# Kernel optimization log

Hardware: AMD Instinct MI355X
Metric: run time of the kernel (lower is better)

The kernel has to match this reference:

```python
import jax, jax.numpy as jnp
import numpy as np

N_NODES = 100000
K_HOPS = 2


def _gcn_norm(edge_index, edge_weight, num_nodes, fill_value=1.0):
    # renorm trick: add self-loops with weight fill_value, then D^-1/2 A D^-1/2
    row, col = edge_index[0], edge_index[1]
    sl = jnp.arange(num_nodes, dtype=edge_index.dtype)
    row = jnp.concatenate([row, sl])
    col = jnp.concatenate([col, sl])
    w = jnp.concatenate([edge_weight, jnp.full((num_nodes,), fill_value, edge_weight.dtype)])
    deg = jax.ops.segment_sum(w, row, num_segments=num_nodes)
    dinv = jnp.where(deg > 0, jax.lax.rsqrt(deg), 0.0)
    normed_w = dinv[row] * w * dinv[col]
    return row, col, normed_w


def setup_inputs() -> dict:
    key = jax.random.key(0)
    k1, k2, k3 = jax.random.split(key, 3)
    n_edges, d, units = 1000000, 64, 64
    x = jax.random.normal(k1, (N_NODES, d), dtype=jnp.float32)
    edge_index = jax.random.randint(k2, (2, n_edges), 0, N_NODES, dtype=jnp.int32)
    edge_weight = jnp.ones((n_edges,), dtype=jnp.float32)
    kernel = jax.random.normal(k3, (d, units), dtype=jnp.float32) * (1.0 / np.sqrt(d))
    bias = jnp.zeros((units,), dtype=jnp.float32)
    return {"x": x, "edge_index": edge_index, "edge_weight": edge_weight,
            "kernel": kernel, "bias": bias}


def reference(x, edge_index, edge_weight, kernel, bias):
    # SGC: K-hop normalized sparse propagation, then single dense linear
    row, col, w = _gcn_norm(edge_index, edge_weight, N_NODES, fill_value=1.0)
    h = x
    for _ in range(K_HOPS):
        h = jax.ops.segment_sum(w[:, None] * h[col], row, num_segments=N_NODES)
    out = h @ kernel + bias  # activation=None
    return out
```

## Files before the change

### kernel.cpp

```cpp
#include <hip/hip_runtime.h>


constexpr int kN = 100000;
constexpr int kD = 64;
constexpr int BSHIFT = 9;
constexpr int NBUCK = (kN + 511) >> BSHIFT;
constexpr int CHUNK = 4096;
constexpr int XW_ROWS = 128;
constexpr int ECW_PAD = 256;

__device__ __forceinline__ float bf2f(unsigned short u) {
    return __uint_as_float(((unsigned)u) << 16);
}
__device__ __forceinline__ unsigned short f2bf(float f) {
    unsigned b = __float_as_uint(f);
    b += 0x7FFF + ((b >> 16) & 1);
    return (unsigned short)(b >> 16);
}

__global__ __launch_bounds__(256) void k_xw_count(const float* __restrict__ x,
                                                  const float* __restrict__ W,
                                                  unsigned short* __restrict__ y,
                                                  const int* __restrict__ row,
                                                  int* __restrict__ bc,
                                                  int nxw, int nblk, int n, int E) {
    __shared__ float Xs[XW_ROWS][kD];
    int bid = blockIdx.x;
    int t = threadIdx.x;
    if (bid >= nxw) {
        int cb = bid - nxw;
        int* hist = (int*)&Xs[0][0];
        hist[t] = 0;
        __syncthreads();
        int g0 = cb * CHUNK;
        int nn = min(CHUNK, E - g0);
        for (int i = t; i < nn; i += 256) {
            atomicAdd(&hist[row[g0 + i] >> BSHIFT], 1);
        }
        __syncthreads();
        if (t < NBUCK) bc[t * nblk + cb] = hist[t];
        return;
    }
    int lane = t & 63;
    int wv = t >> 6;
    int row0 = bid * XW_ROWS;
    float Wc[kD];
#pragma unroll
    for (int k = 0; k < kD; ++k) Wc[k] = W[k * kD + lane];
    for (int i = t; i < XW_ROWS * (kD / 4); i += 256) {
        int r = i >> 4;
        int q = i & 15;
        float4 v = make_float4(0.0f, 0.0f, 0.0f, 0.0f);
        if (row0 + r < n)
            v = *reinterpret_cast<const float4*>(x + (size_t)(row0 + r) * kD + q * 4);
        *reinterpret_cast<float4*>(&Xs[r][q * 4]) = v;
    }
    __syncthreads();
    int rbase = wv * 32;
#pragma unroll
    for (int rr = 0; rr < 32; rr += 2) {
        int r0 = rbase + rr;
        float acc0 = 0.0f, acc1 = 0.0f;
#pragma unroll
        for (int q = 0; q < 16; ++q) {
            float4 a = *reinterpret_cast<const float4*>(&Xs[r0][q * 4]);
            float4 b = *reinterpret_cast<const float4*>(&Xs[r0 + 1][q * 4]);
            acc0 = fmaf(a.x, Wc[q * 4 + 0], acc0);
            acc1 = fmaf(b.x, Wc[q * 4 + 0], acc1);
            acc0 = fmaf(a.y, Wc[q * 4 + 1], acc0);
            acc1 = fmaf(b.y, Wc[q * 4 + 1], acc1);
            acc0 = fmaf(a.z, Wc[q * 4 + 2], acc0);
            acc1 = fmaf(b.z, Wc[q * 4 + 2], acc1);
            acc0 = fmaf(a.w, Wc[q * 4 + 3], acc0);
            acc1 = fmaf(b.w, Wc[q * 4 + 3], acc1);
        }
        int gr = row0 + r0;
        if (gr < n) y[(size_t)gr * kD + lane] = f2bf(acc0);
        if (gr + 1 < n) y[(size_t)(gr + 1) * kD + lane] = f2bf(acc1);
    }
}

__global__ __launch_bounds__(256) void kA_scanB(int* __restrict__ bc,
                                                int* __restrict__ tot, int nblk) {
    __shared__ int sh[256];
    int b = blockIdx.x;
    int t = threadIdx.x;
    int* p = bc + (size_t)b * nblk;
    int ipt = (nblk + 255) >> 8;
    int s0 = t * ipt;
    int s1 = min(s0 + ipt, nblk);
    int lsum = 0;
    for (int k = s0; k < s1; ++k) lsum += p[k];
    sh[t] = lsum;
    __syncthreads();
    for (int off = 1; off < 256; off <<= 1) {
        int add = (t >= off) ? sh[t - off] : 0;
        __syncthreads();
        sh[t] += add;
        __syncthreads();
    }
    int run = sh[t] - lsum;
    for (int k = s0; k < s1; ++k) {
        int v = p[k];
        p[k] = run;
        run += v;
    }
    if (t == 255) tot[b] = sh[255];
}

__global__ __launch_bounds__(256) void kA_scanT(const int* __restrict__ tot,
                                                int* __restrict__ base,
                                                int2* __restrict__ ecw_pad) {
    __shared__ int sh[256];
    int t = threadIdx.x;
    int v = (t < NBUCK) ? tot[t] : 0;
    sh[t] = v;
    __syncthreads();
    for (int off = 1; off < 256; off <<= 1) {
        int add = (t >= off) ? sh[t - off] : 0;
        __syncthreads();
        sh[t] += add;
        __syncthreads();
    }
    if (t < NBUCK) base[t] = sh[t] - v;
    ecw_pad[t] = make_int2(0, 0);
}

__global__ __launch_bounds__(256) void kA_place(const int* __restrict__ row,
                                                const int* __restrict__ col,
                                                const float* __restrict__ w,
                                                const int* __restrict__ bc,
                                                const int* __restrict__ base, int nblk,
                                                int2* __restrict__ tmp, int E) {
    __shared__ int hist[256];
    __shared__ int lbase[256];
    __shared__ int gb[256];
    __shared__ int cur[256];
    __shared__ int2 stage[CHUNK];
    __shared__ unsigned char bkt[CHUNK];
    int t = threadIdx.x;
    hist[t] = 0;
    __syncthreads();
    int g0 = blockIdx.x * CHUNK;
    int n = min(CHUNK, E - g0);
    for (int i = t; i < n; i += 256) {
        atomicAdd(&hist[row[g0 + i] >> BSHIFT], 1);
    }
    __syncthreads();
    int v = hist[t];
    lbase[t] = v;
    __syncthreads();
    for (int off = 1; off < 256; off <<= 1) {
        int add = (t >= off) ? lbase[t - off] : 0;
        __syncthreads();
        lbase[t] += add;
        __syncthreads();
    }
    int excl = lbase[t] - v;
    __syncthreads();
    lbase[t] = excl;
    cur[t] = excl;
    if (t < NBUCK) gb[t] = base[t] + bc[t * nblk + blockIdx.x];
    __syncthreads();
    for (int i = t; i < n; i += 256) {
        int r = row[g0 + i];
        int c = col[g0 + i];
        float wv = w[g0 + i];
        int b = r >> BSHIFT;
        int lp = atomicAdd(&cur[b], 1);
        stage[lp] = make_int2(c | ((r & 511) << 17), __float_as_int(wv));
        bkt[lp] = (unsigned char)b;
    }
    __syncthreads();
    for (int i = t; i < n; i += 256) {
        int b = bkt[i];
        tmp[gb[b] + (i - lbase[b])] = stage[i];
    }
}

__global__ __launch_bounds__(512) void kD_deg(const int2* __restrict__ tmp,
                                              const int* __restrict__ base,
                                              float* __restrict__ dinv, int E) {
    __shared__ float degs[512];
    int b = blockIdx.x;
    int t = threadIdx.x;
    degs[t] = 0.0f;
    __syncthreads();
    int gbase = base[b];
    int gend = (b == NBUCK - 1) ? E : base[b + 1];
    int node0 = b << BSHIFT;
    int nloc = min(512, kN - node0);
    for (int i = gbase + t; i < gend; i += 512) {
        int2 e = tmp[i];
        atomicAdd(&degs[(e.x >> 17) & 511], __int_as_float(e.y));
    }
    __syncthreads();
    if (t < nloc) {
        float d = 1.0f + degs[t];
        dinv[node0 + t] = (d > 0.0f) ? rsqrtf(d) : 0.0f;
    }
}

__global__ __launch_bounds__(512) void kB_sort(const int2* __restrict__ tmp,
                                               const int* __restrict__ base,
                                               const float* __restrict__ dinv,
                                               int2* __restrict__ ecw,
                                               int* __restrict__ start, int E) {
    __shared__ int hist[512];
    __shared__ int cur[512];
    int b = blockIdx.x;
    int t = threadIdx.x;
    int gbase = base[b];
    int gend = (b == NBUCK - 1) ? E : base[b + 1];
    int size = gend - gbase;
    int node0 = b << BSHIFT;
    int nloc = min(512, kN - node0);
    hist[t] = 0;
    __syncthreads();
    for (int i = t; i < size; i += 512) {
        atomicAdd(&hist[(tmp[gbase + i].x >> 17) & 511], 1);
    }
    __syncthreads();
    int v = hist[t];
    hist[t] = v;
    __syncthreads();
    for (int off = 1; off < 512; off <<= 1) {
        int add = (t >= off) ? hist[t - off] : 0;
        __syncthreads();
        hist[t] += add;
        __syncthreads();
    }
    int excl = hist[t] - v;
    __syncthreads();
    cur[t] = excl;
    __syncthreads();
    if (t < nloc) start[node0 + t] = gbase + excl;
    if (b == 0 && t == 0) start[kN] = E;
    for (int i = t; i < size; i += 512) {
        int2 e = tmp[gbase + i];
        int c = e.x & 0x1FFFF;
        int rl = (e.x >> 17) & 511;
        float wn = dinv[node0 + rl] * __int_as_float(e.y) * dinv[c];
        int lp = atomicAdd(&cur[rl], 1);
        ecw[gbase + lp] = make_int2(c << 7, __float_as_int(wn));
    }
}

template <typename OutWriter>
__device__ __forceinline__ void hop_body(const int* __restrict__ start,
                                         const int2* __restrict__ ecw,
                                         const float* __restrict__ dinv,
                                         const unsigned short* __restrict__ h_in,
                                         int n, OutWriter writeout) {
    int wv = threadIdx.x >> 6;
    int lane = threadIdx.x & 63;
    int q = lane >> 4;
    int f = lane & 15;
    int node = blockIdx.x * 16 + wv * 4 + q;
    bool valid = node < n;
    int nd = valid ? node : (n - 1);
    const char* hb = (const char*)h_in;
    int lo = f << 3;
    float di = dinv[nd];
    float d2 = di * di;
    uint2 su = *(const uint2*)(hb + ((size_t)nd << 7) + lo);
    float acc0 = d2 * __uint_as_float(su.x << 16);
    float acc1 = d2 * __uint_as_float(su.x & 0xffff0000u);
    float acc2 = d2 * __uint_as_float(su.y << 16);
    float acc3 = d2 * __uint_as_float(su.y & 0xffff0000u);
    int s = start[nd], e = start[nd + 1];
    int d = e - s;
    int m1 = max(d, __shfl_xor(d, 16));
    int dmax = max(m1, __shfl_xor(m1, 32));
    for (int it = 0; it < dmax; it += 4) {
        int j = s + it;
        int2 v0 = ecw[j + 0];
        int2 v1 = ecw[j + 1];
        int2 v2 = ecw[j + 2];
        int2 v3 = ecw[j + 3];
        uint2 g0 = *(const uint2*)(hb + (unsigned)(v0.x + lo));
        uint2 g1 = *(const uint2*)(hb + (unsigned)(v1.x + lo));
        uint2 g2 = *(const uint2*)(hb + (unsigned)(v2.x + lo));
        uint2 g3 = *(const uint2*)(hb + (unsigned)(v3.x + lo));
        float w0 = (it + 0 < d) ? __int_as_float(v0.y) : 0.0f;
        float w1 = (it + 1 < d) ? __int_as_float(v1.y) : 0.0f;
        float w2 = (it + 2 < d) ? __int_as_float(v2.y) : 0.0f;
        float w3 = (it + 3 < d) ? __int_as_float(v3.y) : 0.0f;
        acc0 = fmaf(w0, __uint_as_float(g0.x << 16), acc0);
        acc1 = fmaf(w0, __uint_as_float(g0.x & 0xffff0000u), acc1);
        acc2 = fmaf(w0, __uint_as_float(g0.y << 16), acc2);
        acc3 = fmaf(w0, __uint_as_float(g0.y & 0xffff0000u), acc3);
        acc0 = fmaf(w1, __uint_as_float(g1.x << 16), acc0);
        acc1 = fmaf(w1, __uint_as_float(g1.x & 0xffff0000u), acc1);
        acc2 = fmaf(w1, __uint_as_float(g1.y << 16), acc2);
        acc3 = fmaf(w1, __uint_as_float(g1.y & 0xffff0000u), acc3);
        acc0 = fmaf(w2, __uint_as_float(g2.x << 16), acc0);
        acc1 = fmaf(w2, __uint_as_float(g2.x & 0xffff0000u), acc1);
        acc2 = fmaf(w2, __uint_as_float(g2.y << 16), acc2);
        acc3 = fmaf(w2, __uint_as_float(g2.y & 0xffff0000u), acc3);
        acc0 = fmaf(w3, __uint_as_float(g3.x << 16), acc0);
        acc1 = fmaf(w3, __uint_as_float(g3.x & 0xffff0000u), acc1);
        acc2 = fmaf(w3, __uint_as_float(g3.y << 16), acc2);
        acc3 = fmaf(w3, __uint_as_float(g3.y & 0xffff0000u), acc3);
    }
    if (valid) writeout(node, f, acc0, acc1, acc2, acc3);
}

__global__ __launch_bounds__(256) void k_hop1(const int* __restrict__ start,
                                              const int2* __restrict__ ecw,
                                              const float* __restrict__ dinv,
                                              const unsigned short* __restrict__ h_in,
                                              uint2* __restrict__ h_out64, int n) {
    hop_body(start, ecw, dinv, h_in, n,
             [=](int node, int f, float a0, float a1, float a2, float a3) {
                 uint2 p;
                 p.x = (unsigned)f2bf(a0) | ((unsigned)f2bf(a1) << 16);
                 p.y = (unsigned)f2bf(a2) | ((unsigned)f2bf(a3) << 16);
                 h_out64[((size_t)node << 4) + f] = p;
             });
}

__global__ __launch_bounds__(256) void k_hop2(const int* __restrict__ start,
                                              const int2* __restrict__ ecw,
                                              const float* __restrict__ dinv,
                                              const unsigned short* __restrict__ h_in,
                                              const float* __restrict__ bias,
                                              float* __restrict__ out, int n) {
    hop_body(start, ecw, dinv, h_in, n,
             [=](int node, int f, float a0, float a1, float a2, float a3) {
                 float4 b = *reinterpret_cast<const float4*>(bias + (f << 2));
                 float4 o = make_float4(a0 + b.x, a1 + b.y, a2 + b.z, a3 + b.w);
                 *reinterpret_cast<float4*>(out + ((size_t)node << 6) + (f << 2)) = o;
             });
}

extern "C" void kernel_launch(void* const* d_in, const int* in_sizes, int n_in,
                              void* d_out, int out_size, void* d_ws, size_t ws_size,
                              hipStream_t stream) {
    const float* x    = (const float*)d_in[0];
    const int*   ei   = (const int*)d_in[1];
    const float* ew   = (const float*)d_in[2];
    const float* W    = (const float*)d_in[3];
    const float* bias = (const float*)d_in[4];
    const int E = in_sizes[1] / 2;
    const int* row = ei;
    const int* col = ei + E;

    const int nblk = (E + CHUNK - 1) / CHUNK;
    const int nxw  = (kN + XW_ROWS - 1) / XW_ROWS;

    char* ws = (char*)d_ws;
    auto alloc = [&](size_t bytes) {
        char* p = ws;
        ws += ((bytes + 1023) & ~(size_t)1023);
        return p;
    };
    int*            base  = (int*)alloc(sizeof(int) * 256);
    int*            tot   = (int*)alloc(sizeof(int) * 256);
    int*            bc    = (int*)alloc(sizeof(int) * (size_t)NBUCK * nblk);
    int*            start = (int*)alloc(sizeof(int) * (kN + 1));
    float*          dinv  = (float*)alloc(sizeof(float) * kN);
    int2*           ecw   = (int2*)alloc(sizeof(int2) * (size_t)(E + ECW_PAD));
    unsigned short* y     = (unsigned short*)alloc(sizeof(short) * (size_t)kN * kD);
    unsigned short* h1    = (unsigned short*)alloc(sizeof(short) * (size_t)kN * kD);
    int2*           tmp   = (int2*)h1;

    k_xw_count<<<nxw + nblk, 256, 0, stream>>>(x, W, y, row, bc, nxw, nblk, kN, E);

    kA_scanB<<<NBUCK, 256, 0, stream>>>(bc, tot, nblk);
    kA_scanT<<<1, 256, 0, stream>>>(tot, base, ecw + E);
    kA_place<<<nblk, 256, 0, stream>>>(row, col, ew, bc, base, nblk, tmp, E);
    kD_deg<<<NBUCK, 512, 0, stream>>>(tmp, base, dinv, E);
    kB_sort<<<NBUCK, 512, 0, stream>>>(tmp, base, dinv, ecw, start, E);

    k_hop1<<<(kN + 15) / 16, 256, 0, stream>>>(start, ecw, dinv, y,
                                               (uint2*)h1, kN);
    k_hop2<<<(kN + 15) / 16, 256, 0, stream>>>(start, ecw, dinv, h1, bias,
                                               (float*)d_out, kN);
}
```

Measured before the change: 123.1 us.

## Widen hop gathers to 16-byte loads and fuse the two scan kernels

The hop kernels now map 8 lanes per node with uint4 (8 bf16) gathers instead of 16 lanes with uint2, so each wave covers 8 nodes and the grid halves. Predicated-off edge offsets are redirected to row 0, which avoids reading invalid addresses. The bucket scan and total scan are merged into one kernel through a last-block-done atomic counter, which removes one launch. The tradeoff is that fewer lanes share each node, so high-degree nodes cause more divergence within a wave, and each thread holds more registers.

```diff
diff --git a/kernel.cpp b/kernel.cpp
--- a/kernel.cpp
+++ b/kernel.cpp
@@ -9,13 +9,16 @@
 constexpr int XW_ROWS = 128;
 constexpr int ECW_PAD = 256;
 
-__device__ __forceinline__ float bf2f(unsigned short u) {
-    return __uint_as_float(((unsigned)u) << 16);
-}
 __device__ __forceinline__ unsigned short f2bf(float f) {
     unsigned b = __float_as_uint(f);
     b += 0x7FFF + ((b >> 16) & 1);
     return (unsigned short)(b >> 16);
+}
+__device__ __forceinline__ float lo16(unsigned u) {
+    return __uint_as_float(u << 16);
+}
+__device__ __forceinline__ float hi16(unsigned u) {
+    return __uint_as_float(u & 0xffff0000u);
 }
 
 __global__ __launch_bounds__(256) void k_xw_count(const float* __restrict__ x,
@@ -23,10 +26,12 @@
                                                   unsigned short* __restrict__ y,
                                                   const int* __restrict__ row,
                                                   int* __restrict__ bc,
+                                                  int* __restrict__ done,
                                                   int nxw, int nblk, int n, int E) {
     __shared__ float Xs[XW_ROWS][kD];
     int bid = blockIdx.x;
     int t = threadIdx.x;
+    if (bid == 0 && t == 0) *done = 0;
     if (bid >= nxw) {
         int cb = bid - nxw;
         int* hist = (int*)&Xs[0][0];
@@ -80,9 +85,13 @@
     }
 }
 
-__global__ __launch_bounds__(256) void kA_scanB(int* __restrict__ bc,
-                                                int* __restrict__ tot, int nblk) {
+__global__ __launch_bounds__(256) void kA_scan(int* __restrict__ bc,
+                                               int* __restrict__ tot,
+                                               int* __restrict__ base,
+                                               int2* __restrict__ ecw_pad,
+                                               int* __restrict__ done, int nblk) {
     __shared__ int sh[256];
+    __shared__ int lastflag;
     int b = blockIdx.x;
     int t = threadIdx.x;
     int* p = bc + (size_t)b * nblk;
@@ -106,24 +115,23 @@
         run += v;
     }
     if (t == 255) tot[b] = sh[255];
-}
-
-__global__ __launch_bounds__(256) void kA_scanT(const int* __restrict__ tot,
-                                                int* __restrict__ base,
-                                                int2* __restrict__ ecw_pad) {
-    __shared__ int sh[256];
-    int t = threadIdx.x;
-    int v = (t < NBUCK) ? tot[t] : 0;
-    sh[t] = v;
-    __syncthreads();
-    for (int off = 1; off < 256; off <<= 1) {
-        int add = (t >= off) ? sh[t - off] : 0;
-        __syncthreads();
-        sh[t] += add;
-        __syncthreads();
-    }
-    if (t < NBUCK) base[t] = sh[t] - v;
-    ecw_pad[t] = make_int2(0, 0);
+    __threadfence();
+    __syncthreads();
+    if (t == 0) lastflag = (atomicAdd(done, 1) == NBUCK - 1);
+    __syncthreads();
+    if (lastflag) {
+        int v = (t < NBUCK) ? atomicAdd(&tot[t], 0) : 0;
+        sh[t] = v;
+        __syncthreads();
+        for (int off = 1; off < 256; off <<= 1) {
+            int add = (t >= off) ? sh[t - off] : 0;
+            __syncthreads();
+            sh[t] += add;
+            __syncthreads();
+        }
+        if (t < NBUCK) base[t] = sh[t] - v;
+        ecw_pad[t] = make_int2(0, 0);
+    }
 }
 
 __global__ __launch_bounds__(256) void kA_place(const int* __restrict__ row,
@@ -254,69 +262,79 @@
                                          int n, OutWriter writeout) {
     int wv = threadIdx.x >> 6;
     int lane = threadIdx.x & 63;
-    int q = lane >> 4;
-    int f = lane & 15;
-    int node = blockIdx.x * 16 + wv * 4 + q;
+    int g = lane >> 3;
+    int f = lane & 7;
+    int node = blockIdx.x * 32 + wv * 8 + g;
     bool valid = node < n;
     int nd = valid ? node : (n - 1);
     const char* hb = (const char*)h_in;
-    int lo = f << 3;
+    int lo = f << 4;
     float di = dinv[nd];
     float d2 = di * di;
-    uint2 su = *(const uint2*)(hb + ((size_t)nd << 7) + lo);
-    float acc0 = d2 * __uint_as_float(su.x << 16);
-    float acc1 = d2 * __uint_as_float(su.x & 0xffff0000u);
-    float acc2 = d2 * __uint_as_float(su.y << 16);
-    float acc3 = d2 * __uint_as_float(su.y & 0xffff0000u);
+    uint4 su = *(const uint4*)(hb + ((size_t)nd << 7) + lo);
+    float a0 = d2 * lo16(su.x), a1 = d2 * hi16(su.x);
+    float a2 = d2 * lo16(su.y), a3 = d2 * hi16(su.y);
+    float a4 = d2 * lo16(su.z), a5 = d2 * hi16(su.z);
+    float a6 = d2 * lo16(su.w), a7 = d2 * hi16(su.w);
     int s = start[nd], e = start[nd + 1];
     int d = e - s;
-    int m1 = max(d, __shfl_xor(d, 16));
-    int dmax = max(m1, __shfl_xor(m1, 32));
+    int m = max(d, __shfl_xor(d, 8));
+    m = max(m, __shfl_xor(m, 16));
+    int dmax = max(m, __shfl_xor(m, 32));
     for (int it = 0; it < dmax; it += 4) {
         int j = s + it;
         int2 v0 = ecw[j + 0];
         int2 v1 = ecw[j + 1];
         int2 v2 = ecw[j + 2];
         int2 v3 = ecw[j + 3];
-        uint2 g0 = *(const uint2*)(hb + (unsigned)(v0.x + lo));
-        uint2 g1 = *(const uint2*)(hb + (unsigned)(v1.x + lo));
-        uint2 g2 = *(const uint2*)(hb + (unsigned)(v2.x + lo));
-        uint2 g3 = *(const uint2*)(hb + (unsigned)(v3.x + lo));
-        float w0 = (it + 0 < d) ? __int_as_float(v0.y) : 0.0f;
-        float w1 = (it + 1 < d) ? __int_as_float(v1.y) : 0.0f;
-        float w2 = (it + 2 < d) ? __int_as_float(v2.y) : 0.0f;
-        float w3 = (it + 3 < d) ? __int_as_float(v3.y) : 0.0f;
-        acc0 = fmaf(w0, __uint_as_float(g0.x << 16), acc0);
-        acc1 = fmaf(w0, __uint_as_float(g0.x & 0xffff0000u), acc1);
-        acc2 = fmaf(w0, __uint_as_float(g0.y << 16), acc2);
-        acc3 = fmaf(w0, __uint_as_float(g0.y & 0xffff0000u), acc3);
-        acc0 = fmaf(w1, __uint_as_float(g1.x << 16), acc0);
-        acc1 = fmaf(w1, __uint_as_float(g1.x & 0xffff0000u), acc1);
-        acc2 = fmaf(w1, __uint_as_float(g1.y << 16), acc2);
-        acc3 = fmaf(w1, __uint_as_float(g1.y & 0xffff0000u), acc3);
-        acc0 = fmaf(w2, __uint_as_float(g2.x << 16), acc0);
-        acc1 = fmaf(w2, __uint_as_float(g2.x & 0xffff0000u), acc1);
-        acc2 = fmaf(w2, __uint_as_float(g2.y << 16), acc2);
-        acc3 = fmaf(w2, __uint_as_float(g2.y & 0xffff0000u), acc3);
-        acc0 = fmaf(w3, __uint_as_float(g3.x << 16), acc0);
-        acc1 = fmaf(w3, __uint_as_float(g3.x & 0xffff0000u), acc1);
-        acc2 = fmaf(w3, __uint_as_float(g3.y << 16), acc2);
-        acc3 = fmaf(w3, __uint_as_float(g3.y & 0xffff0000u), acc3);
-    }
-    if (valid) writeout(node, f, acc0, acc1, acc2, acc3);
+        bool p0 = (it + 0 < d), p1 = (it + 1 < d);
+        bool p2 = (it + 2 < d), p3 = (it + 3 < d);
+        unsigned o0 = p0 ? (unsigned)v0.x : 0u;
+        unsigned o1 = p1 ? (unsigned)v1.x : 0u;
+        unsigned o2 = p2 ? (unsigned)v2.x : 0u;
+        unsigned o3 = p3 ? (unsigned)v3.x : 0u;
+        uint4 g0 = *(const uint4*)(hb + (o0 + lo));
+        uint4 g1 = *(const uint4*)(hb + (o1 + lo));
+        uint4 g2 = *(const uint4*)(hb + (o2 + lo));
+        uint4 g3 = *(const uint4*)(hb + (o3 + lo));
+        float w0 = p0 ? __int_as_float(v0.y) : 0.0f;
+        float w1 = p1 ? __int_as_float(v1.y) : 0.0f;
+        float w2 = p2 ? __int_as_float(v2.y) : 0.0f;
+        float w3 = p3 ? __int_as_float(v3.y) : 0.0f;
+        a0 = fmaf(w0, lo16(g0.x), a0); a1 = fmaf(w0, hi16(g0.x), a1);
+        a2 = fmaf(w0, lo16(g0.y), a2); a3 = fmaf(w0, hi16(g0.y), a3);
+        a4 = fmaf(w0, lo16(g0.z), a4); a5 = fmaf(w0, hi16(g0.z), a5);
+        a6 = fmaf(w0, lo16(g0.w), a6); a7 = fmaf(w0, hi16(g0.w), a7);
+        a0 = fmaf(w1, lo16(g1.x), a0); a1 = fmaf(w1, hi16(g1.x), a1);
+        a2 = fmaf(w1, lo16(g1.y), a2); a3 = fmaf(w1, hi16(g1.y), a3);
+        a4 = fmaf(w1, lo16(g1.z), a4); a5 = fmaf(w1, hi16(g1.z), a5);
+        a6 = fmaf(w1, lo16(g1.w), a6); a7 = fmaf(w1, hi16(g1.w), a7);
+        a0 = fmaf(w2, lo16(g2.x), a0); a1 = fmaf(w2, hi16(g2.x), a1);
+        a2 = fmaf(w2, lo16(g2.y), a2); a3 = fmaf(w2, hi16(g2.y), a3);
+        a4 = fmaf(w2, lo16(g2.z), a4); a5 = fmaf(w2, hi16(g2.z), a5);
+        a6 = fmaf(w2, lo16(g2.w), a6); a7 = fmaf(w2, hi16(g2.w), a7);
+        a0 = fmaf(w3, lo16(g3.x), a0); a1 = fmaf(w3, hi16(g3.x), a1);
+        a2 = fmaf(w3, lo16(g3.y), a2); a3 = fmaf(w3, hi16(g3.y), a3);
+        a4 = fmaf(w3, lo16(g3.z), a4); a5 = fmaf(w3, hi16(g3.z), a5);
+        a6 = fmaf(w3, lo16(g3.w), a6); a7 = fmaf(w3, hi16(g3.w), a7);
+    }
+    if (valid) writeout(node, f, a0, a1, a2, a3, a4, a5, a6, a7);
 }
 
 __global__ __launch_bounds__(256) void k_hop1(const int* __restrict__ start,
                                               const int2* __restrict__ ecw,
                                               const float* __restrict__ dinv,
                                               const unsigned short* __restrict__ h_in,
-                                              uint2* __restrict__ h_out64, int n) {
+                                              uint4* __restrict__ h_out, int n) {
     hop_body(start, ecw, dinv, h_in, n,
-             [=](int node, int f, float a0, float a1, float a2, float a3) {
-                 uint2 p;
+             [=](int node, int f, float a0, float a1, float a2, float a3,
+                 float a4, float a5, float a6, float a7) {
+                 uint4 p;
                  p.x = (unsigned)f2bf(a0) | ((unsigned)f2bf(a1) << 16);
                  p.y = (unsigned)f2bf(a2) | ((unsigned)f2bf(a3) << 16);
-                 h_out64[((size_t)node << 4) + f] = p;
+                 p.z = (unsigned)f2bf(a4) | ((unsigned)f2bf(a5) << 16);
+                 p.w = (unsigned)f2bf(a6) | ((unsigned)f2bf(a7) << 16);
+                 h_out[((size_t)node << 3) + f] = p;
              });
 }
 
@@ -327,10 +345,13 @@
                                               const float* __restrict__ bias,
                                               float* __restrict__ out, int n) {
     hop_body(start, ecw, dinv, h_in, n,
-             [=](int node, int f, float a0, float a1, float a2, float a3) {
-                 float4 b = *reinterpret_cast<const float4*>(bias + (f << 2));
-                 float4 o = make_float4(a0 + b.x, a1 + b.y, a2 + b.z, a3 + b.w);
-                 *reinterpret_cast<float4*>(out + ((size_t)node << 6) + (f << 2)) = o;
+             [=](int node, int f, float a0, float a1, float a2, float a3,
+                 float a4, float a5, float a6, float a7) {
+                 const float4* bp = reinterpret_cast<const float4*>(bias + (f << 3));
+                 float4 b0 = bp[0], b1 = bp[1];
+                 float4* op = reinterpret_cast<float4*>(out + ((size_t)node << 6) + (f << 3));
+                 op[0] = make_float4(a0 + b0.x, a1 + b0.y, a2 + b0.z, a3 + b0.w);
+                 op[1] = make_float4(a4 + b1.x, a5 + b1.y, a6 + b1.z, a7 + b1.w);
              });
 }
 
@@ -357,6 +378,7 @@
     };
     int*            base  = (int*)alloc(sizeof(int) * 256);
     int*            tot   = (int*)alloc(sizeof(int) * 256);
+    int*            done  = (int*)alloc(sizeof(int) * 64);
     int*            bc    = (int*)alloc(sizeof(int) * (size_t)NBUCK * nblk);
     int*            start = (int*)alloc(sizeof(int) * (kN + 1));
     float*          dinv  = (float*)alloc(sizeof(float) * kN);
@@ -365,16 +387,16 @@
     unsigned short* h1    = (unsigned short*)alloc(sizeof(short) * (size_t)kN * kD);
     int2*           tmp   = (int2*)h1;
 
-    k_xw_count<<<nxw + nblk, 256, 0, stream>>>(x, W, y, row, bc, nxw, nblk, kN, E);
-
-    kA_scanB<<<NBUCK, 256, 0, stream>>>(bc, tot, nblk);
-    kA_scanT<<<1, 256, 0, stream>>>(tot, base, ecw + E);
+    k_xw_count<<<nxw + nblk, 256, 0, stream>>>(x, W, y, row, bc, done,
+                                               nxw, nblk, kN, E);
+
+    kA_scan<<<NBUCK, 256, 0, stream>>>(bc, tot, base, ecw + E, done, nblk);
     kA_place<<<nblk, 256, 0, stream>>>(row, col, ew, bc, base, nblk, tmp, E);
     kD_deg<<<NBUCK, 512, 0, stream>>>(tmp, base, dinv, E);
     kB_sort<<<NBUCK, 512, 0, stream>>>(tmp, base, dinv, ecw, start, E);
 
-    k_hop1<<<(kN + 15) / 16, 256, 0, stream>>>(start, ecw, dinv, y,
-                                               (uint2*)h1, kN);
-    k_hop2<<<(kN + 15) / 16, 256, 0, stream>>>(start, ecw, dinv, h1, bias,
+    k_hop1<<<(kN + 31) / 32, 256, 0, stream>>>(start, ecw, dinv, y,
+                                               (uint4*)h1, kN);
+    k_hop2<<<(kN + 31) / 32, 256, 0, stream>>>(start, ecw, dinv, h1, bias,
                                                (float*)d_out, kN);
 }
```

Result: slower. 130.3 us (+5.8%).
